# Optimization experiments

Hardware: AMD Instinct MI355X
Metric: run time of the kernel (lower is better)

Reference implementation:

```python
import jax, jax.numpy as jnp
import numpy as np
import math

D_MODEL = 1024
N_HEADS = 16
RANK = 256  # int(d_model * 0.25)
RANK_PER_HEAD = RANK // N_HEADS  # 16
HEAD_DIM = D_MODEL // N_HEADS  # 64
B, L = 32, 512


def setup_inputs() -> dict:
    key = jax.random.key(0)
    kx, kq, kk, kv, ku, kvv = jax.random.split(key, 6)
    x = jax.random.normal(kx, (B, L, D_MODEL), dtype=jnp.float32)
    mask = jnp.ones((B, L), dtype=bool)
    s = 1.0 / math.sqrt(D_MODEL)
    Wq = jax.random.normal(kq, (RANK, D_MODEL), dtype=jnp.float32) * s
    Wk = jax.random.normal(kk, (RANK, D_MODEL), dtype=jnp.float32) * s
    Wv = jax.random.normal(kv, (RANK, D_MODEL), dtype=jnp.float32) * s
    # xavier_uniform for U [H, head_dim, r_h] and V [H, r_h, head_dim]
    lim = math.sqrt(6.0 / (HEAD_DIM + RANK_PER_HEAD))
    U = jax.random.uniform(ku, (N_HEADS, HEAD_DIM, RANK_PER_HEAD), jnp.float32, -lim, lim)
    V = jax.random.uniform(kvv, (N_HEADS, RANK_PER_HEAD, HEAD_DIM), jnp.float32, -lim, lim)
    return {"x": x, "mask": mask, "Wq": Wq, "Wk": Wk, "Wv": Wv, "U": U, "V": V}


def _rope_tables(seq_len, head_dim, dtype):
    half = head_dim // 2
    theta = 1.0 / (10000.0 ** (jnp.arange(half, dtype=jnp.float32) / half))
    freqs = jnp.arange(seq_len, dtype=jnp.float32)[:, None] * theta[None, :]  # [L, half]
    return jnp.cos(freqs).astype(dtype), jnp.sin(freqs).astype(dtype)


def _apply_rope(x, cos, sin):
    # x: [B, L, H, D]; complex multiply on interleaved pairs
    Bq, Lq, H, D = x.shape
    xr = x.reshape(Bq, Lq, H, D // 2, 2)
    x0, x1 = xr[..., 0], xr[..., 1]
    c = cos[None, :, None, :]
    s = sin[None, :, None, :]
    o0 = x0 * c - x1 * s
    o1 = x0 * s + x1 * c
    return jnp.stack([o0, o1], axis=-1).reshape(Bq, Lq, H, D)


def reference(x, mask, Wq, Wk, Wv, U, V):
    Bq, Lq, _ = x.shape
    H, head_dim, r_h = U.shape
    q_low = (x @ Wq.T).reshape(Bq, Lq, H, r_h)
    k_low = (x @ Wk.T).reshape(Bq, Lq, H, r_h)
    v_low = (x @ Wv.T).reshape(Bq, Lq, H, r_h)
    q = jnp.einsum('hdr,blhr->blhd', U, q_low)
    k = jnp.einsum('hdr,blhr->blhd', U, k_low)
    cos, sin = _rope_tables(Lq, head_dim, x.dtype)
    q = _apply_rope(q, cos, sin)
    k = _apply_rope(k, cos, sin)
    attn = jnp.einsum('blhd,bmhd->bhlm', q, k) / math.sqrt(head_dim)
    attn = jnp.where(mask[:, None, None, :], attn, -jnp.inf)
    attn = jax.nn.softmax(attn, axis=-1)
    out = jnp.einsum('bhlm,bmhr->blhr', attn, v_low)
    out = jnp.einsum('blhr,hrd->blhd', out, V)
    return out.reshape(Bq, Lq, H * head_dim)
```

## Files before the change

### kernel.cpp

```cpp
#include <hip/hip_runtime.h>
#include <hip/hip_bf16.h>

#define B_   32
#define L_   512
#define DM_  1024
#define H_   16
#define RH_  16
#define HD_  64
#define NTOK (B_ * L_)

typedef short s16x8 __attribute__((ext_vector_type(8)));
typedef float f32x4 __attribute__((ext_vector_type(4)));
#define MFMA16(a,b,c) __builtin_amdgcn_mfma_f32_16x16x32_bf16(a, b, c, 0, 0, 0)

#define GLOAD_LDS16(g, l) __builtin_amdgcn_global_load_lds( \
    (const __attribute__((address_space(1))) unsigned int*)(g), \
    (__attribute__((address_space(3))) unsigned int*)(l), 16, 0, 0)

__device__ inline ushort f2bf(float f) {
    unsigned u = __builtin_bit_cast(unsigned, f);
    u += 0x7fffu + ((u >> 16) & 1u);
    return (ushort)(u >> 16);
}
__device__ inline float bf2f(ushort u) {
    return __builtin_bit_cast(float, (unsigned)u << 16);
}

__global__ __launch_bounds__(256) void cvt_x(const float* __restrict__ src,
                                             ushort* __restrict__ dst) {
    const size_t i = ((size_t)blockIdx.x * 256 + threadIdx.x) * 8;
    float4 a = *(const float4*)(src + i);
    float4 b = *(const float4*)(src + i + 4);
    ushort o[8] = {f2bf(a.x), f2bf(a.y), f2bf(a.z), f2bf(a.w),
                   f2bf(b.x), f2bf(b.y), f2bf(b.z), f2bf(b.w)};
    *(uint4*)(dst + i) = *(const uint4*)o;
}

__global__ __launch_bounds__(256) void cvt_w(const float* __restrict__ Wq,
                                             const float* __restrict__ Wk,
                                             const float* __restrict__ Wv,
                                             ushort* __restrict__ dst) {
    const size_t i = ((size_t)blockIdx.x * 256 + threadIdx.x) * 8;
    const size_t sz = 256 * 1024;
    const float* src = (i < sz) ? (Wq + i) : (i < 2 * sz) ? (Wk + i - sz)
                                                          : (Wv + i - 2 * sz);
    float4 a = *(const float4*)(src);
    float4 b = *(const float4*)(src + 4);
    ushort o[8] = {f2bf(a.x), f2bf(a.y), f2bf(a.z), f2bf(a.w),
                   f2bf(b.x), f2bf(b.y), f2bf(b.z), f2bf(b.w)};
    *(uint4*)(dst + i) = *(const uint4*)o;
}

__global__ __launch_bounds__(256) void proj_mfma(
    const ushort* __restrict__ A,
    const ushort* __restrict__ Bm,
    float* __restrict__ C)
{
    const int bm = blockIdx.x;
    const int bn = blockIdx.y;
    const int tid = threadIdx.x;
    const int lane = tid & 63;
    const int ln15 = lane & 15, quad = lane >> 4;
    const int w = tid >> 6, wy = w >> 1, wx = w & 1;

    __shared__ ushort As[128 * 64];
    __shared__ ushort Bs[128 * 64];

    const int srow = tid >> 3;
    const int gch  = (tid & 7) ^ (srow & 7);
    const ushort* Ag = A + ((size_t)(bm * 128 + srow)) * DM_ + gch * 8;
    const ushort* Bg = Bm + ((size_t)(bn * 128 + srow)) * DM_ + gch * 8;
    ushort* Al = As + tid * 8;
    ushort* Bl = Bs + tid * 8;

    f32x4 acc[4][4] = {};

    for (int kt = 0; kt < DM_ / 64; ++kt) {
        __syncthreads();
        const int ko = kt * 64;
        #pragma unroll
        for (int i = 0; i < 4; ++i) {
            GLOAD_LDS16(Ag + (size_t)(i * 32) * DM_ + ko, Al + i * 2048);
            GLOAD_LDS16(Bg + (size_t)(i * 32) * DM_ + ko, Bl + i * 2048);
        }
        __syncthreads();

        s16x8 Af[4][2], Bf[4][2];
        #pragma unroll
        for (int i = 0; i < 4; ++i) {
            const int m = wy * 64 + i * 16 + ln15;
            const int n = wx * 64 + i * 16 + ln15;
            #pragma unroll
            for (int kh = 0; kh < 2; ++kh) {
                const int c = kh * 4 + quad;
                Af[i][kh] = *(const s16x8*)&As[m * 64 + ((c ^ (m & 7)) * 8)];
                Bf[i][kh] = *(const s16x8*)&Bs[n * 64 + ((c ^ (n & 7)) * 8)];
            }
        }
        #pragma unroll
        for (int i = 0; i < 4; ++i)
            #pragma unroll
            for (int j = 0; j < 4; ++j) {
                acc[i][j] = MFMA16(Af[i][0], Bf[j][0], acc[i][j]);
                acc[i][j] = MFMA16(Af[i][1], Bf[j][1], acc[i][j]);
            }
    }

    #pragma unroll
    for (int i = 0; i < 4; ++i) {
        #pragma unroll
        for (int r = 0; r < 4; ++r) {
            const int grow = bm * 128 + wy * 64 + i * 16 + quad * 4 + r;
            float* cp = C + (size_t)grow * 768 + bn * 128 + wx * 64 + ln15;
            #pragma unroll
            for (int j = 0; j < 4; ++j)
                cp[j * 16] = acc[i][j][r];
        }
    }
}

#define USTRIDE 1032
#define VSTRIDE 520

__global__ __launch_bounds__(512) void expand_rope(
    const float* __restrict__ low,
    const float* __restrict__ U,
    ushort* __restrict__ qr,
    ushort* __restrict__ kr,
    ushort* __restrict__ vt)
{
    const int blk = blockIdx.x;
    const int b   = blk >> 4;
    const int l0  = (blk & 15) * 32;
    const int tid = threadIdx.x;
    const int h   = tid & 15;
    const int tok = tid >> 4;
    const int l   = l0 + tok;
    const int t   = b * L_ + l;

    __shared__ ushort Uls[16 * USTRIDE];
    __shared__ ushort vst[16 * VSTRIDE];

    float ql[16], kl[16], vl[16];
    {
        const float* lp = low + (size_t)t * 768 + h * 16;
        #pragma unroll
        for (int j = 0; j < 4; ++j) {
            float4 a = *(const float4*)(lp + j * 4);
            float4 c = *(const float4*)(lp + 256 + j * 4);
            float4 v = *(const float4*)(lp + 512 + j * 4);
            ql[j*4+0]=a.x; ql[j*4+1]=a.y; ql[j*4+2]=a.z; ql[j*4+3]=a.w;
            kl[j*4+0]=c.x; kl[j*4+1]=c.y; kl[j*4+2]=c.z; kl[j*4+3]=c.w;
            vl[j*4+0]=v.x; vl[j*4+1]=v.y; vl[j*4+2]=v.z; vl[j*4+3]=v.w;
        }
    }

    #pragma unroll
    for (int k = 0; k < 8; ++k) {
        const int e4 = tid + k * 512;
        float4 u4 = ((const float4*)U)[e4];
        const int g = e4 * 4;
        const int hh = g >> 10, off = g & 1023;
        ushort o[4] = {f2bf(u4.x), f2bf(u4.y), f2bf(u4.z), f2bf(u4.w)};
        *(ushort4*)&Uls[hh * USTRIDE + off] = *(const ushort4*)o;
    }
    __syncthreads();

    #pragma unroll
    for (int r = 0; r < 16; ++r)
        vst[h * VSTRIDE + r * 32 + tok] = f2bf(vl[r]);

    const ushort* Uh = &Uls[h * USTRIDE];
    ushort* qp = qr + (((size_t)(b * H_ + h) * L_) + l) * HD_;
    ushort* kp = kr + (((size_t)(b * H_ + h) * L_) + l) * HD_;
    const float L2C = 13.287712379549449f / 32.0f;

    #pragma unroll
    for (int ch = 0; ch < 8; ++ch) {
        float qv[8], kv[8];
        #pragma unroll
        for (int d = 0; d < 8; ++d) {
            const int dd = ch * 8 + d;
            s16x8 u0 = *(const s16x8*)&Uh[dd * 16];
            s16x8 u1 = *(const s16x8*)&Uh[dd * 16 + 8];
            float s1 = 0.f, s2 = 0.f;
            #pragma unroll
            for (int r = 0; r < 8; ++r) {
                const float uf = bf2f((ushort)u0[r]);
                s1 = fmaf(uf, ql[r], s1);
                s2 = fmaf(uf, kl[r], s2);
            }
            #pragma unroll
            for (int r = 0; r < 8; ++r) {
                const float uf = bf2f((ushort)u1[r]);
                s1 = fmaf(uf, ql[8 + r], s1);
                s2 = fmaf(uf, kl[8 + r], s2);
            }
            qv[d] = s1; kv[d] = s2;
        }
        #pragma unroll
        for (int pj = 0; pj < 4; ++pj) {
            const int i = ch * 4 + pj;
            const float ang = (float)l * exp2f(-(float)i * L2C);
            const float c = __cosf(ang), s = __sinf(ang);
            float x0 = qv[2*pj], x1 = qv[2*pj+1];
            qv[2*pj]   = x0 * c - x1 * s;
            qv[2*pj+1] = x0 * s + x1 * c;
            x0 = kv[2*pj]; x1 = kv[2*pj+1];
            kv[2*pj]   = x0 * c - x1 * s;
            kv[2*pj+1] = x0 * s + x1 * c;
        }
        ushort qo[8], ko[8];
        #pragma unroll
        for (int d = 0; d < 8; ++d) {
            qo[d] = f2bf(qv[d] * 0.125f);
            ko[d] = f2bf(kv[d]);
        }
        *(uint4*)(qp + ch * 8) = *(const uint4*)qo;
        *(uint4*)(kp + ch * 8) = *(const uint4*)ko;
    }

    __syncthreads();

    #pragma unroll
    for (int k = 0; k < 2; ++k) {
        const int c = tid + k * 512;
        const int hh = c >> 6, rr = (c >> 2) & 15, j = c & 3;
        uint4 v = *(const uint4*)&vst[hh * VSTRIDE + rr * 32 + j * 8];
        *(uint4*)&vt[(((size_t)(b * H_ + hh) * RH_) + rr) * L_ + l0 + j * 8] = v;
    }
}

__global__ __launch_bounds__(256) void attn_mfma(
    const ushort* __restrict__ qr,
    const ushort* __restrict__ kr,
    const ushort* __restrict__ vt,
    const float*  __restrict__ V,
    float* __restrict__ out)
{
    const int gid = blockIdx.x;
    const int bh = ((gid >> 6) << 3) | (gid & 7);
    const int qt = (gid >> 3) & 7;
    const int b = bh >> 4, h = bh & 15;
    const int tid = threadIdx.x;
    const int w = tid >> 6, lane = tid & 63;
    const int ln15 = lane & 15, quad = lane >> 4;

    __shared__ ushort Ks[2][64 * 64];
    __shared__ ushort Vts[2][16 * 64];
    __shared__ ushort Pb[4][16 * 64];
    __shared__ float  VhS[16 * 64];

    *(float4*)&VhS[tid * 4] = *(const float4*)(V + (size_t)h * RH_ * HD_ + tid * 4);

    const ushort* qbase = qr + ((size_t)bh * L_ + qt * 64 + w * 16 + ln15) * HD_;
    s16x8 Qf0 = *(const s16x8*)(qbase + quad * 8);
    s16x8 Qf1 = *(const s16x8*)(qbase + 32 + quad * 8);

    const ushort* kbase = kr + (size_t)bh * L_ * HD_;
    const ushort* vbase = vt + (size_t)bh * RH_ * L_;

    float lsum = 0.f;
    f32x4 Oacc = {0.f, 0.f, 0.f, 0.f};

    auto stage = [&](int c, int buf) {
        #pragma unroll
        for (int i = 0; i < 2; ++i) {
            const int f = tid + i * 256;
            const int key = f >> 3, ch = f & 7;
            GLOAD_LDS16(kbase + (size_t)(c * 64 + key) * HD_ + ((ch ^ (key & 7)) * 8),
                        &Ks[buf][f * 8]);
        }
        if (w < 2) {
            const int f = tid;
            const int r = f >> 3, ch = f & 7;
            GLOAD_LDS16(vbase + (size_t)r * L_ + c * 64 + ((ch ^ (r & 7)) * 8),
                        &Vts[buf][f * 8]);
        }
    };

    stage(0, 0);
    __syncthreads();

    for (int c = 0; c < 8; ++c) {
        const int cur = c & 1;
        if (c < 7) stage(c + 1, cur ^ 1);

        f32x4 Sc[4];
        #pragma unroll
        for (int ct = 0; ct < 4; ++ct) {
            const int key = ln15 + 16 * ct;
            s16x8 k0 = *(const s16x8*)&Ks[cur][key * 64 + ((quad ^ (key & 7)) * 8)];
            s16x8 k1 = *(const s16x8*)&Ks[cur][key * 64 + (((4 + quad) ^ (key & 7)) * 8)];
            f32x4 acc = {0.f, 0.f, 0.f, 0.f};
            acc = MFMA16(k0, Qf0, acc);
            acc = MFMA16(k1, Qf1, acc);
            Sc[ct] = acc;
        }

        ushort* pb = Pb[w];
        float tsum = 0.f;
        #pragma unroll
        for (int ct = 0; ct < 4; ++ct) {
            const float p0 = __expf(Sc[ct][0]);
            const float p1 = __expf(Sc[ct][1]);
            const float p2 = __expf(Sc[ct][2]);
            const float p3 = __expf(Sc[ct][3]);
            tsum += (p0 + p1) + (p2 + p3);
            uint2 pk;
            pk.x = (unsigned)f2bf(p0) | ((unsigned)f2bf(p1) << 16);
            pk.y = (unsigned)f2bf(p2) | ((unsigned)f2bf(p3) << 16);
            const int key0 = ct * 16 + quad * 4;
            const int chp = key0 >> 3, kop = key0 & 7;
            *(uint2*)&pb[ln15 * 64 + ((chp ^ (ln15 & 7)) * 8) + kop] = pk;
        }
        lsum += tsum;

        asm volatile("s_waitcnt lgkmcnt(0)" ::: "memory");
        __builtin_amdgcn_sched_barrier(0);

        #pragma unroll
        for (int half = 0; half < 2; ++half) {
            const int ch = half * 4 + quad;
            s16x8 pa = *(const s16x8*)&pb[ln15 * 64 + ((ch ^ (ln15 & 7)) * 8)];
            s16x8 vb = *(const s16x8*)&Vts[cur][ln15 * 64 + ((ch ^ (ln15 & 7)) * 8)];
            Oacc = MFMA16(pa, vb, Oacc);
        }

        __syncthreads();
    }

    lsum += __shfl_xor(lsum, 16, 64);
    lsum += __shfl_xor(lsum, 32, 64);
    const float inv = 1.0f / lsum;

    float* Olds = (float*)Pb[w];
    #pragma unroll
    for (int r = 0; r < 4; ++r) {
        const float li = __shfl(inv, quad * 4 + r, 64);
        Olds[(quad * 4 + r) * 16 + ln15] = Oacc[r] * li;
    }
    asm volatile("s_waitcnt lgkmcnt(0)" ::: "memory");
    __builtin_amdgcn_sched_barrier(0);

    const int q = lane >> 2, dc = lane & 3;
    float orow[16];
    #pragma unroll
    for (int j = 0; j < 4; ++j) {
        float4 o4 = *(const float4*)&Olds[q * 16 + j * 4];
        orow[j * 4 + 0] = o4.x; orow[j * 4 + 1] = o4.y;
        orow[j * 4 + 2] = o4.z; orow[j * 4 + 3] = o4.w;
    }
    float4 res[4] = {};
    #pragma unroll
    for (int r = 0; r < 16; ++r) {
        const float ov = orow[r];
        #pragma unroll
        for (int j = 0; j < 4; ++j) {
            float4 v4 = *(const float4*)&VhS[r * 64 + dc * 16 + j * 4];
            res[j].x = fmaf(ov, v4.x, res[j].x);
            res[j].y = fmaf(ov, v4.y, res[j].y);
            res[j].z = fmaf(ov, v4.z, res[j].z);
            res[j].w = fmaf(ov, v4.w, res[j].w);
        }
    }
    const int l = qt * 64 + w * 16 + q;
    float* op = out + (((size_t)b * L_ + l) * H_ + h) * HD_ + dc * 16;
    #pragma unroll
    for (int j = 0; j < 4; ++j)
        *(float4*)(op + j * 4) = res[j];
}

extern "C" void kernel_launch(void* const* d_in, const int* in_sizes, int n_in,
                              void* d_out, int out_size, void* d_ws, size_t ws_size,
                              hipStream_t stream) {
    const float* x  = (const float*)d_in[0];
    const float* Wq = (const float*)d_in[2];
    const float* Wk = (const float*)d_in[3];
    const float* Wv = (const float*)d_in[4];
    const float* U  = (const float*)d_in[5];
    const float* V  = (const float*)d_in[6];
    float* out = (float*)d_out;

    float*  low = (float*)d_ws;
    ushort* Wb  = (ushort*)(low + (size_t)NTOK * 768);
    ushort* vtb = Wb + (size_t)768 * DM_;
    ushort* qrb = vtb + (size_t)B_ * H_ * RH_ * L_;
    ushort* krb = qrb + (size_t)B_ * H_ * L_ * HD_;
    ushort* xb  = qrb;

    cvt_x<<<NTOK * DM_ / (256 * 8), 256, 0, stream>>>(x, xb);
    cvt_w<<<768 * DM_ / (256 * 8), 256, 0, stream>>>(Wq, Wk, Wv, Wb);
    proj_mfma<<<dim3(NTOK / 128, 768 / 128), 256, 0, stream>>>(xb, Wb, low);
    expand_rope<<<512, 512, 0, stream>>>(low, U, qrb, krb, vtb);
    attn_mfma<<<B_ * H_ * 8, 256, 0, stream>>>(qrb, krb, vtb, V, out);
}
```

Baseline: 281.1 us.

## Fuse x fp32-to-bf16 conversion into projection GEMM with register prefetch

Drops the separate cvt_x kernel. The projection GEMM now reads fp32 x directly, converts it to bf16 in registers and writes the result to LDS, while the next k-tile of x is prefetched into registers during the MFMA compute. This removes a full 64 MB fp32 read plus a 32 MB bf16 write/read round trip through global memory. In exchange, the GEMM reads x in fp32 six times (once per N-block of the grid), and register pressure rises from the prefetch buffers.

```diff
diff --git a/kernel.cpp b/kernel.cpp
--- a/kernel.cpp
+++ b/kernel.cpp
@@ -24,16 +24,6 @@
 }
 __device__ inline float bf2f(ushort u) {
     return __builtin_bit_cast(float, (unsigned)u << 16);
-}
-
-__global__ __launch_bounds__(256) void cvt_x(const float* __restrict__ src,
-                                             ushort* __restrict__ dst) {
-    const size_t i = ((size_t)blockIdx.x * 256 + threadIdx.x) * 8;
-    float4 a = *(const float4*)(src + i);
-    float4 b = *(const float4*)(src + i + 4);
-    ushort o[8] = {f2bf(a.x), f2bf(a.y), f2bf(a.z), f2bf(a.w),
-                   f2bf(b.x), f2bf(b.y), f2bf(b.z), f2bf(b.w)};
-    *(uint4*)(dst + i) = *(const uint4*)o;
 }
 
 __global__ __launch_bounds__(256) void cvt_w(const float* __restrict__ Wq,
@@ -52,7 +42,7 @@
 }
 
 __global__ __launch_bounds__(256) void proj_mfma(
-    const ushort* __restrict__ A,
+    const float*  __restrict__ X,
     const ushort* __restrict__ Bm,
     float* __restrict__ C)
 {
@@ -68,22 +58,39 @@
 
     const int srow = tid >> 3;
     const int gch  = (tid & 7) ^ (srow & 7);
-    const ushort* Ag = A + ((size_t)(bm * 128 + srow)) * DM_ + gch * 8;
+    const float*  Ag = X  + ((size_t)(bm * 128 + srow)) * DM_ + gch * 8;
     const ushort* Bg = Bm + ((size_t)(bn * 128 + srow)) * DM_ + gch * 8;
     ushort* Al = As + tid * 8;
     ushort* Bl = Bs + tid * 8;
 
     f32x4 acc[4][4] = {};
 
+    float4 pa0[4], pa1[4];
+    #pragma unroll
+    for (int i = 0; i < 4; ++i) {
+        pa0[i] = *(const float4*)(Ag + (size_t)(i * 32) * DM_);
+        pa1[i] = *(const float4*)(Ag + (size_t)(i * 32) * DM_ + 4);
+    }
+
     for (int kt = 0; kt < DM_ / 64; ++kt) {
         __syncthreads();
-        const int ko = kt * 64;
         #pragma unroll
         for (int i = 0; i < 4; ++i) {
-            GLOAD_LDS16(Ag + (size_t)(i * 32) * DM_ + ko, Al + i * 2048);
-            GLOAD_LDS16(Bg + (size_t)(i * 32) * DM_ + ko, Bl + i * 2048);
+            ushort o[8] = {f2bf(pa0[i].x), f2bf(pa0[i].y), f2bf(pa0[i].z), f2bf(pa0[i].w),
+                           f2bf(pa1[i].x), f2bf(pa1[i].y), f2bf(pa1[i].z), f2bf(pa1[i].w)};
+            *(uint4*)(Al + i * 2048) = *(const uint4*)o;
+            GLOAD_LDS16(Bg + (size_t)(i * 32) * DM_ + kt * 64, Bl + i * 2048);
         }
         __syncthreads();
+
+        if (kt < DM_ / 64 - 1) {
+            const int ko = (kt + 1) * 64;
+            #pragma unroll
+            for (int i = 0; i < 4; ++i) {
+                pa0[i] = *(const float4*)(Ag + (size_t)(i * 32) * DM_ + ko);
+                pa1[i] = *(const float4*)(Ag + (size_t)(i * 32) * DM_ + ko + 4);
+            }
+        }
 
         s16x8 Af[4][2], Bf[4][2];
         #pragma unroll
@@ -387,11 +394,9 @@
     ushort* vtb = Wb + (size_t)768 * DM_;
     ushort* qrb = vtb + (size_t)B_ * H_ * RH_ * L_;
     ushort* krb = qrb + (size_t)B_ * H_ * L_ * HD_;
-    ushort* xb  = qrb;
-
-    cvt_x<<<NTOK * DM_ / (256 * 8), 256, 0, stream>>>(x, xb);
+
     cvt_w<<<768 * DM_ / (256 * 8), 256, 0, stream>>>(Wq, Wk, Wv, Wb);
-    proj_mfma<<<dim3(NTOK / 128, 768 / 128), 256, 0, stream>>>(xb, Wb, low);
+    proj_mfma<<<dim3(NTOK / 128, 768 / 128), 256, 0, stream>>>(x, Wb, low);
     expand_rope<<<512, 512, 0, stream>>>(low, U, qrb, krb, vtb);
     attn_mfma<<<B_ * H_ * 8, 256, 0, stream>>>(qrb, krb, vtb, V, out);
 }
```

Result: no change. 282.5 us (+0.5%).
